# Kernel optimization log

Measured on AMD Instinct MI355X. Metric: run time of the kernel, lower is better.

The kernel has to match this reference:

```python
import jax, jax.numpy as jnp
import numpy as np

B, S, D = 16, 577, 768      # batch, BLIP vision tokens (1 CLS + 576 patches), hidden
C, NCLS = 256, 1000         # num_concepts, num_classes
TOPK = 16


def setup_inputs() -> dict:
    key = jax.random.key(0)
    k1, k2, k3 = jax.random.split(key, 3)
    q = jax.random.normal(k1, (B, S, D), dtype=jnp.float32)          # BLIP last_hidden_state
    concept_w = jax.random.normal(k2, (C, D), dtype=jnp.float32) * 0.02  # nn.Embedding weight
    cls_w = jax.random.normal(k3, (NCLS, D), dtype=jnp.float32) * 0.02   # nn.Linear weight
    cls_b = jnp.zeros((NCLS,), dtype=jnp.float32)
    return {"q": q, "concept_w": concept_w, "cls_w": cls_w, "cls_b": cls_b, "topk": TOPK}


def reference(q, concept_w, cls_w, cls_b, topk):
    qp = q[:, 1:]                                             # [B, S-1, D] drop CLS token
    qk = jnp.einsum('bsd,cd->bcs', qp, concept_w)             # [B, C, S-1] concept similarities
    qk_topk, idx_topk = jax.lax.top_k(qk, topk)               # [B, C, K]
    # batched gather: q_topk[b,c,k] = qp[b, idx_topk[b,c,k]]
    q_topk = jnp.take_along_axis(qp[:, None], idx_topk[..., None], axis=2)  # [B, C, K, D]
    score = jax.nn.softmax(qk_topk, axis=2)                   # [B, C, K]
    h = (q_topk * score[..., None]).sum(axis=2).mean(axis=1)  # [B, D]
    y = jax.nn.relu(h) @ cls_w.T + cls_b                      # [B, NCLS]
    return y
```

## Files before the change

kernel.cpp:

```cpp
#include <hip/hip_runtime.h>

#define NB 16
#define S_TOK 577
#define SP 576
#define DIM 768
#define NC 256
#define NCLS 1000
#define TK 16
#define HCH 6
#define HCHS 96

typedef __attribute__((ext_vector_type(8))) __bf16 bf16x8;
typedef __attribute__((ext_vector_type(4))) float f32x4;

__device__ __forceinline__ void cvt_split(const float4 a, const float4 b,
                                          bf16x8& hi, bf16x8& lo) {
  float v[8] = {a.x, a.y, a.z, a.w, b.x, b.y, b.z, b.w};
#pragma unroll
  for (int i = 0; i < 8; i++) {
    __bf16 h = (__bf16)v[i];
    hi[i] = h;
    lo[i] = (__bf16)(v[i] - (float)h);
  }
}

__device__ __forceinline__ bf16x8 frag_ld(const char* base, int r, int kc) {
  return *(const bf16x8*)(base + ((r * 4 + (kc ^ (r & 3))) << 4));
}

__global__ __launch_bounds__(256) void qk_gemm_mfma(const float* __restrict__ q,
                                                    const float* __restrict__ cw,
                                                    float* __restrict__ qk, int b0) {
  const int bl = blockIdx.z;
  const int s0 = blockIdx.x * 64;
  const int c0 = blockIdx.y * 64;
  __shared__ __align__(16) char sAH[4096], sAL[4096], sBH[4096], sBL[4096];

  const int tid = threadIdx.x;
  const int lane = tid & 63;
  const int wid = tid >> 6;
  const int wc = (wid >> 1) << 5;
  const int wsv = (wid & 1) << 5;
  const int fr = lane & 15;
  const int kq = lane >> 4;

  const int r = tid >> 2;
  const int ck = tid & 3;
  const int wslot = (r * 4 + (ck ^ (r & 3))) << 4;

  const float* qb = q + ((size_t)(b0 + bl) * S_TOK + 1) * DIM;
  const float* arow = cw + (size_t)(c0 + r) * DIM + ck * 8;
  const float* brow = qb + (size_t)(s0 + r) * DIM + ck * 8;

  f32x4 zero = {0.f, 0.f, 0.f, 0.f};
  f32x4 acc[2][2];
#pragma unroll
  for (int i = 0; i < 2; i++)
#pragma unroll
    for (int j = 0; j < 2; j++) acc[i][j] = zero;

  for (int k0 = 0; k0 < DIM; k0 += 32) {
    float4 a0 = *(const float4*)(arow + k0);
    float4 a1 = *(const float4*)(arow + k0 + 4);
    float4 b0v = *(const float4*)(brow + k0);
    float4 b1v = *(const float4*)(brow + k0 + 4);
    __syncthreads();
    bf16x8 h, l;
    cvt_split(a0, a1, h, l);
    *(bf16x8*)(sAH + wslot) = h;
    *(bf16x8*)(sAL + wslot) = l;
    cvt_split(b0v, b1v, h, l);
    *(bf16x8*)(sBH + wslot) = h;
    *(bf16x8*)(sBL + wslot) = l;
    __syncthreads();
    bf16x8 a0h = frag_ld(sAH, wc + fr, kq);
    bf16x8 a0l = frag_ld(sAL, wc + fr, kq);
    bf16x8 a1h = frag_ld(sAH, wc + 16 + fr, kq);
    bf16x8 a1l = frag_ld(sAL, wc + 16 + fr, kq);
    bf16x8 b0h = frag_ld(sBH, wsv + fr, kq);
    bf16x8 b0l = frag_ld(sBL, wsv + fr, kq);
    bf16x8 b1h = frag_ld(sBH, wsv + 16 + fr, kq);
    bf16x8 b1l = frag_ld(sBL, wsv + 16 + fr, kq);
#define MF(A, B, C) C = __builtin_amdgcn_mfma_f32_16x16x32_bf16(A, B, C, 0, 0, 0)
    MF(a0h, b0h, acc[0][0]); MF(a0h, b0l, acc[0][0]); MF(a0l, b0h, acc[0][0]);
    MF(a0h, b1h, acc[0][1]); MF(a0h, b1l, acc[0][1]); MF(a0l, b1h, acc[0][1]);
    MF(a1h, b0h, acc[1][0]); MF(a1h, b0l, acc[1][0]); MF(a1l, b0h, acc[1][0]);
    MF(a1h, b1h, acc[1][1]); MF(a1h, b1l, acc[1][1]); MF(a1l, b1h, acc[1][1]);
#undef MF
  }
  float* obase = qk + (size_t)bl * NC * SP;
#pragma unroll
  for (int i = 0; i < 2; i++)
#pragma unroll
    for (int j = 0; j < 2; j++)
#pragma unroll
      for (int rr = 0; rr < 4; rr++) {
        const int row = c0 + wc + i * 16 + kq * 4 + rr;
        const int col = s0 + wsv + j * 16 + fr;
        obase[(size_t)row * SP + col] = acc[i][j][rr];
      }
}

__global__ __launch_bounds__(256) void topk_store(const float* __restrict__ qk,
                                                  float* __restrict__ score,
                                                  int* __restrict__ sidx, int b0) {
  const int lane = threadIdx.x & 63;
  const int wid = threadIdx.x >> 6;
  const int rcl = blockIdx.x * 4 + wid;
  const int bl = rcl >> 8;
  const int c = rcl & 255;
  const float* rowp = qk + (size_t)rcl * SP;
  float v[9];
#pragma unroll
  for (int j = 0; j < 9; j++) v[j] = rowp[lane + 64 * j];

  float vals[TK];
  int idxs[TK];
#pragma unroll
  for (int t = 0; t < TK; t++) {
    float bv = -1e30f;
    int bj = 0;
#pragma unroll
    for (int j = 0; j < 9; j++)
      if (v[j] > bv) { bv = v[j]; bj = j; }
    int bs = lane + 64 * bj;
#pragma unroll
    for (int off = 32; off >= 1; off >>= 1) {
      float ov = __shfl_xor(bv, off);
      int os = __shfl_xor(bs, off);
      if (ov > bv || (ov == bv && os < bs)) { bv = ov; bs = os; }
    }
    vals[t] = bv;
    idxs[t] = bs;
    const int clr_j = bs >> 6;
    const int clr_lane = bs & 63;
#pragma unroll
    for (int j = 0; j < 9; j++)
      if (j == clr_j && clr_lane == lane) v[j] = -1e30f;
  }
  float m = vals[0];
  float sum = 0.f;
#pragma unroll
  for (int t = 0; t < TK; t++) sum += expf(vals[t] - m);
  if (lane == 0) {
    const float inv = 1.f / (sum * (float)NC);
    const size_t base = ((size_t)(b0 + bl) * NC + c) * TK;
#pragma unroll
    for (int t = 0; t < TK; t++) {
      score[base + t] = expf(vals[t] - m) * inv;
      sidx[base + t] = idxs[t];
    }
  }
}

__global__ __launch_bounds__(256) void w_build(const float* __restrict__ score,
                                               const int* __restrict__ sidx,
                                               float* __restrict__ W) {
  const int b = blockIdx.x;
  __shared__ float Ws[SP];
  for (int i = threadIdx.x; i < SP; i += 256) Ws[i] = 0.f;
  __syncthreads();
  const size_t base = (size_t)b * NC * TK;
  for (int i = threadIdx.x; i < NC * TK; i += 256)
    atomicAdd(&Ws[sidx[base + i]], score[base + i]);
  __syncthreads();
  for (int i = threadIdx.x; i < SP; i += 256) W[b * SP + i] = Ws[i];
}

__global__ __launch_bounds__(256) void h_partial(const float* __restrict__ q,
                                                 const float* __restrict__ W,
                                                 float* __restrict__ hpart) {
  const int b = blockIdx.y;
  const int ch = blockIdx.z;
  const int d = blockIdx.x * 256 + threadIdx.x;
  __shared__ float Ws[HCHS];
  if (threadIdx.x < HCHS) Ws[threadIdx.x] = W[b * SP + ch * HCHS + threadIdx.x];
  __syncthreads();
  const float* qb = q + ((size_t)b * S_TOK + 1 + ch * HCHS) * DIM + d;
  float acc = 0.f;
#pragma unroll 8
  for (int s = 0; s < HCHS; s++) acc = fmaf(Ws[s], qb[(size_t)s * DIM], acc);
  hpart[((size_t)ch * NB + b) * DIM + d] = acc;
}

__global__ __launch_bounds__(256) void cls_head(const float* __restrict__ hp,
                                                const float* __restrict__ cw,
                                                const float* __restrict__ cb,
                                                float* __restrict__ y) {
  __shared__ float hs[NB * DIM];
  for (int i = threadIdx.x; i < NB * DIM; i += 256) {
    float s = 0.f;
#pragma unroll
    for (int ch = 0; ch < HCH; ch++) s += hp[(size_t)ch * NB * DIM + i];
    hs[i] = fmaxf(s, 0.f);
  }
  __syncthreads();
  const int lane = threadIdx.x & 63;
  const int n = blockIdx.x * 4 + (threadIdx.x >> 6);
  float wr[12];
#pragma unroll
  for (int j = 0; j < 12; j++) wr[j] = cw[(size_t)n * DIM + lane + 64 * j];
  const float bias = cb[n];
  for (int bb = 0; bb < NB; bb++) {
    float dot = 0.f;
#pragma unroll
    for (int j = 0; j < 12; j++)
      dot = fmaf(wr[j], hs[bb * DIM + lane + 64 * j], dot);
#pragma unroll
    for (int off = 32; off >= 1; off >>= 1) dot += __shfl_xor(dot, off);
    if (lane == 0) y[bb * NCLS + n] = dot + bias;
  }
}

extern "C" void kernel_launch(void* const* d_in, const int* in_sizes, int n_in,
                              void* d_out, int out_size, void* d_ws, size_t ws_size,
                              hipStream_t stream) {
  const float* q = (const float*)d_in[0];
  const float* cw = (const float*)d_in[1];
  const float* clsw = (const float*)d_in[2];
  const float* clsb = (const float*)d_in[3];
  float* out = (float*)d_out;

  float* score = (float*)d_ws;
  int* sidx = (int*)(score + (size_t)NB * NC * TK);
  float* W = (float*)(sidx + (size_t)NB * NC * TK);
  float* hpart = W + (size_t)NB * SP;
  float* qk = hpart + (size_t)HCH * NB * DIM;
  const size_t aux_bytes = (size_t)((char*)qk - (char*)d_ws);

  int bper = NB;
  while (bper > 1 &&
         aux_bytes + (size_t)bper * NC * SP * sizeof(float) > ws_size)
    bper >>= 1;

  for (int b0 = 0; b0 < NB; b0 += bper) {
    qk_gemm_mfma<<<dim3(9, 4, bper), 256, 0, stream>>>(q, cw, qk, b0);
    topk_store<<<(bper * NC) / 4, 256, 0, stream>>>(qk, score, sidx, b0);
  }
  w_build<<<NB, 256, 0, stream>>>(score, sidx, W);
  h_partial<<<dim3(3, NB, HCH), 256, 0, stream>>>(q, W, hpart);
  cls_head<<<NCLS / 4, 256, 0, stream>>>(hpart, clsw, clsb, out);
}
```

Measured before the change: 76.66 us.

## Enlarge GEMM concept tile and fuse W scatter into top-k via global atomics

The QK GEMM tile grows from 64x64 to 128x64 along concepts, so each block computes 4x2 MFMA fragments and reuses each loaded q tile across twice as many concepts. This halves the number of blocks and the redundant loads and bf16 split conversions of q. The separate w_build kernel and its score/index buffers are removed: top-k now adds softmax weights directly into W with global atomicAdd, and the GEMM kernel zeroes W. The larger tile lowers the block count to 288 and raises register pressure, and global atomics make the summation order nondeterministic.

After: 73.88 us. 3.6% less time.

```diff
diff --git a/kernel.cpp b/kernel.cpp
--- a/kernel.cpp
+++ b/kernel.cpp
@@ -30,67 +30,88 @@
 
 __global__ __launch_bounds__(256) void qk_gemm_mfma(const float* __restrict__ q,
                                                     const float* __restrict__ cw,
-                                                    float* __restrict__ qk, int b0) {
+                                                    float* __restrict__ qk,
+                                                    float* __restrict__ W, int b0) {
   const int bl = blockIdx.z;
   const int s0 = blockIdx.x * 64;
-  const int c0 = blockIdx.y * 64;
-  __shared__ __align__(16) char sAH[4096], sAL[4096], sBH[4096], sBL[4096];
+  const int c0 = blockIdx.y * 128;
+  __shared__ __align__(16) char sAH[8192], sAL[8192], sBH[4096], sBL[4096];
+
+  if (blockIdx.x == 0 && blockIdx.y == 0) {
+    for (int i = threadIdx.x; i < SP; i += 256) W[(b0 + bl) * SP + i] = 0.f;
+  }
 
   const int tid = threadIdx.x;
   const int lane = tid & 63;
   const int wid = tid >> 6;
-  const int wc = (wid >> 1) << 5;
+  const int wc = (wid >> 1) << 6;
   const int wsv = (wid & 1) << 5;
   const int fr = lane & 15;
   const int kq = lane >> 4;
 
-  const int r = tid >> 2;
-  const int ck = tid & 3;
-  const int wslot = (r * 4 + (ck ^ (r & 3))) << 4;
+  const int ra0 = (tid * 2) >> 2, cka0 = (tid * 2) & 3;
+  const int ra1 = (tid * 2 + 1) >> 2, cka1 = (tid * 2 + 1) & 3;
+  const int rb = tid >> 2, ckb = tid & 3;
+  const int slotA0 = (ra0 * 4 + (cka0 ^ (ra0 & 3))) << 4;
+  const int slotA1 = (ra1 * 4 + (cka1 ^ (ra1 & 3))) << 4;
+  const int slotB = (rb * 4 + (ckb ^ (rb & 3))) << 4;
 
   const float* qb = q + ((size_t)(b0 + bl) * S_TOK + 1) * DIM;
-  const float* arow = cw + (size_t)(c0 + r) * DIM + ck * 8;
-  const float* brow = qb + (size_t)(s0 + r) * DIM + ck * 8;
+  const float* arow0 = cw + (size_t)(c0 + ra0) * DIM + cka0 * 8;
+  const float* arow1 = cw + (size_t)(c0 + ra1) * DIM + cka1 * 8;
+  const float* brow = qb + (size_t)(s0 + rb) * DIM + ckb * 8;
 
   f32x4 zero = {0.f, 0.f, 0.f, 0.f};
-  f32x4 acc[2][2];
-#pragma unroll
-  for (int i = 0; i < 2; i++)
+  f32x4 acc[4][2];
+#pragma unroll
+  for (int i = 0; i < 4; i++)
 #pragma unroll
     for (int j = 0; j < 2; j++) acc[i][j] = zero;
 
   for (int k0 = 0; k0 < DIM; k0 += 32) {
-    float4 a0 = *(const float4*)(arow + k0);
-    float4 a1 = *(const float4*)(arow + k0 + 4);
+    float4 a00 = *(const float4*)(arow0 + k0);
+    float4 a01 = *(const float4*)(arow0 + k0 + 4);
+    float4 a10 = *(const float4*)(arow1 + k0);
+    float4 a11 = *(const float4*)(arow1 + k0 + 4);
     float4 b0v = *(const float4*)(brow + k0);
     float4 b1v = *(const float4*)(brow + k0 + 4);
     __syncthreads();
     bf16x8 h, l;
-    cvt_split(a0, a1, h, l);
-    *(bf16x8*)(sAH + wslot) = h;
-    *(bf16x8*)(sAL + wslot) = l;
+    cvt_split(a00, a01, h, l);
+    *(bf16x8*)(sAH + slotA0) = h;
+    *(bf16x8*)(sAL + slotA0) = l;
+    cvt_split(a10, a11, h, l);
+    *(bf16x8*)(sAH + slotA1) = h;
+    *(bf16x8*)(sAL + slotA1) = l;
     cvt_split(b0v, b1v, h, l);
-    *(bf16x8*)(sBH + wslot) = h;
-    *(bf16x8*)(sBL + wslot) = l;
+    *(bf16x8*)(sBH + slotB) = h;
+    *(bf16x8*)(sBL + slotB) = l;
     __syncthreads();
-    bf16x8 a0h = frag_ld(sAH, wc + fr, kq);
-    bf16x8 a0l = frag_ld(sAL, wc + fr, kq);
-    bf16x8 a1h = frag_ld(sAH, wc + 16 + fr, kq);
-    bf16x8 a1l = frag_ld(sAL, wc + 16 + fr, kq);
-    bf16x8 b0h = frag_ld(sBH, wsv + fr, kq);
-    bf16x8 b0l = frag_ld(sBL, wsv + fr, kq);
-    bf16x8 b1h = frag_ld(sBH, wsv + 16 + fr, kq);
-    bf16x8 b1l = frag_ld(sBL, wsv + 16 + fr, kq);
+    bf16x8 ah[4], al[4], bh[2], blo[2];
+#pragma unroll
+    for (int i = 0; i < 4; i++) {
+      ah[i] = frag_ld(sAH, wc + i * 16 + fr, kq);
+      al[i] = frag_ld(sAL, wc + i * 16 + fr, kq);
+    }
+#pragma unroll
+    for (int j = 0; j < 2; j++) {
+      bh[j] = frag_ld(sBH, wsv + j * 16 + fr, kq);
+      blo[j] = frag_ld(sBL, wsv + j * 16 + fr, kq);
+    }
 #define MF(A, B, C) C = __builtin_amdgcn_mfma_f32_16x16x32_bf16(A, B, C, 0, 0, 0)
-    MF(a0h, b0h, acc[0][0]); MF(a0h, b0l, acc[0][0]); MF(a0l, b0h, acc[0][0]);
-    MF(a0h, b1h, acc[0][1]); MF(a0h, b1l, acc[0][1]); MF(a0l, b1h, acc[0][1]);
-    MF(a1h, b0h, acc[1][0]); MF(a1h, b0l, acc[1][0]); MF(a1l, b0h, acc[1][0]);
-    MF(a1h, b1h, acc[1][1]); MF(a1h, b1l, acc[1][1]); MF(a1l, b1h, acc[1][1]);
+#pragma unroll
+    for (int i = 0; i < 4; i++)
+#pragma unroll
+      for (int j = 0; j < 2; j++) {
+        MF(ah[i], bh[j], acc[i][j]);
+        MF(ah[i], blo[j], acc[i][j]);
+        MF(al[i], bh[j], acc[i][j]);
+      }
 #undef MF
   }
   float* obase = qk + (size_t)bl * NC * SP;
 #pragma unroll
-  for (int i = 0; i < 2; i++)
+  for (int i = 0; i < 4; i++)
 #pragma unroll
     for (int j = 0; j < 2; j++)
 #pragma unroll
@@ -101,14 +122,13 @@
       }
 }
 
-__global__ __launch_bounds__(256) void topk_store(const float* __restrict__ qk,
-                                                  float* __restrict__ score,
-                                                  int* __restrict__ sidx, int b0) {
+__global__ __launch_bounds__(256) void topk_scatter(const float* __restrict__ qk,
+                                                    float* __restrict__ W, int b0) {
   const int lane = threadIdx.x & 63;
   const int wid = threadIdx.x >> 6;
   const int rcl = blockIdx.x * 4 + wid;
   const int bl = rcl >> 8;
-  const int c = rcl & 255;
+  const int b = b0 + bl;
   const float* rowp = qk + (size_t)rcl * SP;
   float v[9];
 #pragma unroll
@@ -144,27 +164,10 @@
   for (int t = 0; t < TK; t++) sum += expf(vals[t] - m);
   if (lane == 0) {
     const float inv = 1.f / (sum * (float)NC);
-    const size_t base = ((size_t)(b0 + bl) * NC + c) * TK;
-#pragma unroll
-    for (int t = 0; t < TK; t++) {
-      score[base + t] = expf(vals[t] - m) * inv;
-      sidx[base + t] = idxs[t];
-    }
-  }
-}
-
-__global__ __launch_bounds__(256) void w_build(const float* __restrict__ score,
-                                               const int* __restrict__ sidx,
-                                               float* __restrict__ W) {
-  const int b = blockIdx.x;
-  __shared__ float Ws[SP];
-  for (int i = threadIdx.x; i < SP; i += 256) Ws[i] = 0.f;
-  __syncthreads();
-  const size_t base = (size_t)b * NC * TK;
-  for (int i = threadIdx.x; i < NC * TK; i += 256)
-    atomicAdd(&Ws[sidx[base + i]], score[base + i]);
-  __syncthreads();
-  for (int i = threadIdx.x; i < SP; i += 256) W[b * SP + i] = Ws[i];
+#pragma unroll
+    for (int t = 0; t < TK; t++)
+      atomicAdd(&W[b * SP + idxs[t]], expf(vals[t] - m) * inv);
+  }
 }
 
 __global__ __launch_bounds__(256) void h_partial(const float* __restrict__ q,
@@ -221,9 +224,7 @@
   const float* clsb = (const float*)d_in[3];
   float* out = (float*)d_out;
 
-  float* score = (float*)d_ws;
-  int* sidx = (int*)(score + (size_t)NB * NC * TK);
-  float* W = (float*)(sidx + (size_t)NB * NC * TK);
+  float* W = (float*)d_ws;
   float* hpart = W + (size_t)NB * SP;
   float* qk = hpart + (size_t)HCH * NB * DIM;
   const size_t aux_bytes = (size_t)((char*)qk - (char*)d_ws);
@@ -234,10 +235,9 @@
     bper >>= 1;
 
   for (int b0 = 0; b0 < NB; b0 += bper) {
-    qk_gemm_mfma<<<dim3(9, 4, bper), 256, 0, stream>>>(q, cw, qk, b0);
-    topk_store<<<(bper * NC) / 4, 256, 0, stream>>>(qk, score, sidx, b0);
-  }
-  w_build<<<NB, 256, 0, stream>>>(score, sidx, W);
+    qk_gemm_mfma<<<dim3(9, 2, bper), 256, 0, stream>>>(q, cw, qk, W, b0);
+    topk_scatter<<<(bper * NC) / 4, 256, 0, stream>>>(qk, W, b0);
+  }
   h_partial<<<dim3(3, NB, HCH), 256, 0, stream>>>(q, W, hpart);
   cls_head<<<NCLS / 4, 256, 0, stream>>>(hpart, clsw, clsb, out);
 }
```

## Fuse per-tile top-k into QK GEMM epilogue and merge candidates with atomic scatter

Applied to the files above, without the earlier changes.

The GEMM kernel no longer writes the full [B,C,576] similarity matrix. Each 64x64 output tile is staged in shared memory and reduced to the top 16 entries per concept row, giving 9 candidate lists per row. A second kernel merges the 144 candidates per row, applies the softmax, and atomically adds the scores into the per-token weight vector W. The W-zeroing moves into the GEMM kernel, which removes the separate w_build kernel. This cuts global traffic for the large intermediate and removes one launch, but the GEMM epilogue now runs 16 serial wave-wide shuffle reductions for each of 16 rows per wave, roughly nine times the original top-k selection work.

After: 218.7 us. 185% more time.

```diff
diff --git a/kernel.cpp b/kernel.cpp
--- a/kernel.cpp
+++ b/kernel.cpp
@@ -9,6 +9,8 @@
 #define TK 16
 #define HCH 6
 #define HCHS 96
+#define NSB 9
+#define NCAND (NSB * TK)
 
 typedef __attribute__((ext_vector_type(8))) __bf16 bf16x8;
 typedef __attribute__((ext_vector_type(4))) float f32x4;
@@ -28,13 +30,21 @@
   return *(const bf16x8*)(base + ((r * 4 + (kc ^ (r & 3))) << 4));
 }
 
-__global__ __launch_bounds__(256) void qk_gemm_mfma(const float* __restrict__ q,
-                                                    const float* __restrict__ cw,
-                                                    float* __restrict__ qk, int b0) {
-  const int bl = blockIdx.z;
-  const int s0 = blockIdx.x * 64;
+__global__ __launch_bounds__(256) void gemm_topk64(const float* __restrict__ q,
+                                                   const float* __restrict__ cw,
+                                                   float* __restrict__ cand,
+                                                   int* __restrict__ candi,
+                                                   float* __restrict__ W) {
+  const int b = blockIdx.z;
+  const int sb = blockIdx.x;
+  const int s0 = sb * 64;
   const int c0 = blockIdx.y * 64;
   __shared__ __align__(16) char sAH[4096], sAL[4096], sBH[4096], sBL[4096];
+  __shared__ float tkbuf[64][65];
+
+  if (blockIdx.x == 0 && blockIdx.y == 0) {
+    for (int i = threadIdx.x; i < SP; i += 256) W[b * SP + i] = 0.f;
+  }
 
   const int tid = threadIdx.x;
   const int lane = tid & 63;
@@ -48,7 +58,7 @@
   const int ck = tid & 3;
   const int wslot = (r * 4 + (ck ^ (r & 3))) << 4;
 
-  const float* qb = q + ((size_t)(b0 + bl) * S_TOK + 1) * DIM;
+  const float* qb = q + ((size_t)b * S_TOK + 1) * DIM;
   const float* arow = cw + (size_t)(c0 + r) * DIM + ck * 8;
   const float* brow = qb + (size_t)(s0 + r) * DIM + ck * 8;
 
@@ -88,55 +98,79 @@
     MF(a1h, b1h, acc[1][1]); MF(a1h, b1l, acc[1][1]); MF(a1l, b1h, acc[1][1]);
 #undef MF
   }
-  float* obase = qk + (size_t)bl * NC * SP;
+
+  __syncthreads();
 #pragma unroll
   for (int i = 0; i < 2; i++)
 #pragma unroll
     for (int j = 0; j < 2; j++)
 #pragma unroll
-      for (int rr = 0; rr < 4; rr++) {
-        const int row = c0 + wc + i * 16 + kq * 4 + rr;
-        const int col = s0 + wsv + j * 16 + fr;
-        obase[(size_t)row * SP + col] = acc[i][j][rr];
+      for (int rr = 0; rr < 4; rr++)
+        tkbuf[wc + i * 16 + kq * 4 + rr][wsv + j * 16 + fr] = acc[i][j][rr];
+  __syncthreads();
+
+  for (int rr2 = 0; rr2 < 16; ++rr2) {
+    const int row = wid * 16 + rr2;
+    float v = tkbuf[row][lane];
+    const size_t obase = ((size_t)(b * NC + c0 + row)) * NCAND + sb * TK;
+    for (int t = 0; t < TK; t++) {
+      float bv = v;
+      int bs = lane;
+#pragma unroll
+      for (int off = 32; off >= 1; off >>= 1) {
+        float ov = __shfl_xor(bv, off);
+        int os = __shfl_xor(bs, off);
+        if (ov > bv || (ov == bv && os < bs)) { bv = ov; bs = os; }
       }
-}
-
-__global__ __launch_bounds__(256) void topk_store(const float* __restrict__ qk,
-                                                  float* __restrict__ score,
-                                                  int* __restrict__ sidx, int b0) {
+      if (lane == 0) {
+        cand[obase + t] = bv;
+        candi[obase + t] = s0 + bs;
+      }
+      if (lane == bs) v = -1e30f;
+    }
+  }
+}
+
+__global__ __launch_bounds__(256) void merge_scatter(const float* __restrict__ cand,
+                                                     const int* __restrict__ candi,
+                                                     float* __restrict__ W) {
   const int lane = threadIdx.x & 63;
   const int wid = threadIdx.x >> 6;
-  const int rcl = blockIdx.x * 4 + wid;
-  const int bl = rcl >> 8;
-  const int c = rcl & 255;
-  const float* rowp = qk + (size_t)rcl * SP;
-  float v[9];
-#pragma unroll
-  for (int j = 0; j < 9; j++) v[j] = rowp[lane + 64 * j];
-
+  const int rc = blockIdx.x * 4 + wid;
+  const int b = rc >> 8;
+  float v[3];
+  int vi[3];
+#pragma unroll
+  for (int j = 0; j < 3; j++) {
+    const int idx = lane + 64 * j;
+    if (idx < NCAND) {
+      v[j] = cand[(size_t)rc * NCAND + idx];
+      vi[j] = candi[(size_t)rc * NCAND + idx];
+    } else {
+      v[j] = -1e30f;
+      vi[j] = 0x7fffffff;
+    }
+  }
   float vals[TK];
   int idxs[TK];
 #pragma unroll
   for (int t = 0; t < TK; t++) {
-    float bv = -1e30f;
-    int bj = 0;
-#pragma unroll
-    for (int j = 0; j < 9; j++)
-      if (v[j] > bv) { bv = v[j]; bj = j; }
-    int bs = lane + 64 * bj;
+    float bv = v[0];
+    int bi = vi[0];
+#pragma unroll
+    for (int j = 1; j < 3; j++)
+      if (v[j] > bv || (v[j] == bv && vi[j] < bi)) { bv = v[j]; bi = vi[j]; }
 #pragma unroll
     for (int off = 32; off >= 1; off >>= 1) {
       float ov = __shfl_xor(bv, off);
-      int os = __shfl_xor(bs, off);
-      if (ov > bv || (ov == bv && os < bs)) { bv = ov; bs = os; }
+      int oi = __shfl_xor(bi, off);
+      if (ov > bv || (ov == bv && oi < bi)) { bv = ov; bi = oi; }
     }
     vals[t] = bv;
-    idxs[t] = bs;
-    const int clr_j = bs >> 6;
-    const int clr_lane = bs & 63;
-#pragma unroll
-    for (int j = 0; j < 9; j++)
-      if (j == clr_j && clr_lane == lane) v[j] = -1e30f;
+    idxs[t] = bi;
+#pragma unroll
+    for (int j = 0; j < 3; j++)
+      if (vi[j] == bi) v[j] = -1e30f;
   }
   float m = vals[0];
   float sum = 0.f;
@@ -144,27 +178,10 @@
   for (int t = 0; t < TK; t++) sum += expf(vals[t] - m);
   if (lane == 0) {
     const float inv = 1.f / (sum * (float)NC);
-    const size_t base = ((size_t)(b0 + bl) * NC + c) * TK;
-#pragma unroll
-    for (int t = 0; t < TK; t++) {
-      score[base + t] = expf(vals[t] - m) * inv;
-      sidx[base + t] = idxs[t];
-    }
-  }
-}
-
-__global__ __launch_bounds__(256) void w_build(const float* __restrict__ score,
-                                               const int* __restrict__ sidx,
-                                               float* __restrict__ W) {
-  const int b = blockIdx.x;
-  __shared__ float Ws[SP];
-  for (int i = threadIdx.x; i < SP; i += 256) Ws[i] = 0.f;
-  __syncthreads();
-  const size_t base = (size_t)b * NC * TK;
-  for (int i = threadIdx.x; i < NC * TK; i += 256)
-    atomicAdd(&Ws[sidx[base + i]], score[base + i]);
-  __syncthreads();
-  for (int i = threadIdx.x; i < SP; i += 256) W[b * SP + i] = Ws[i];
+#pragma unroll
+    for (int t = 0; t < TK; t++)
+      atomicAdd(&W[b * SP + idxs[t]], expf(vals[t] - m) * inv);
+  }
 }
 
 __global__ __launch_bounds__(256) void h_partial(const float* __restrict__ q,
@@ -221,23 +238,13 @@
   const float* clsb = (const float*)d_in[3];
   float* out = (float*)d_out;
 
-  float* score = (float*)d_ws;
-  int* sidx = (int*)(score + (size_t)NB * NC * TK);
-  float* W = (float*)(sidx + (size_t)NB * NC * TK);
+  float* W = (float*)d_ws;
   float* hpart = W + (size_t)NB * SP;
-  float* qk = hpart + (size_t)HCH * NB * DIM;
-  const size_t aux_bytes = (size_t)((char*)qk - (char*)d_ws);
-
-  int bper = NB;
-  while (bper > 1 &&
-         aux_bytes + (size_t)bper * NC * SP * sizeof(float) > ws_size)
-    bper >>= 1;
-
-  for (int b0 = 0; b0 < NB; b0 += bper) {
-    qk_gemm_mfma<<<dim3(9, 4, bper), 256, 0, stream>>>(q, cw, qk, b0);
-    topk_store<<<(bper * NC) / 4, 256, 0, stream>>>(qk, score, sidx, b0);
-  }
-  w_build<<<NB, 256, 0, stream>>>(score, sidx, W);
+  float* cand = hpart + (size_t)HCH * NB * DIM;
+  int* candi = (int*)(cand + (size_t)NB * NC * NCAND);
+
+  gemm_topk64<<<dim3(NSB, 4, NB), 256, 0, stream>>>(q, cw, cand, candi, W);
+  merge_scatter<<<(NB * NC) / 4, 256, 0, stream>>>(cand, candi, W);
   h_partial<<<dim3(3, NB, HCH), 256, 0, stream>>>(q, W, hpart);
   cls_head<<<NCLS / 4, 256, 0, stream>>>(hpart, clsw, clsb, out);
 }
```
